# Optimization experiments

Measured on AMD Instinct MI355X. Metric: run time of the kernel, lower is better.

The kernel has to match this reference:

```python
import jax, jax.numpy as jnp
import numpy as np

MARGIN = 0.2
ENCODER_STRIDE = 320


def setup_inputs() -> dict:
    key = jax.random.key(0)
    k1, k2, k3, k4 = jax.random.split(key, 4)
    B, D, T, NC = 8, 512, 2048, 4096
    student_features = jax.random.normal(k1, (B, D, T), dtype=jnp.float32)
    codebook = jax.random.normal(k2, (NC, D), dtype=jnp.float32)
    teacher_codes = jax.random.randint(k3, (B, T), 0, NC, dtype=jnp.int64)
    lengths = jax.random.randint(k4, (B,), 0, T * ENCODER_STRIDE, dtype=jnp.int64)
    return {
        "student_features": student_features,
        "teacher_codes": teacher_codes,
        "codebook": codebook,
        "lengths": lengths,
    }


def reference(student_features, teacher_codes, codebook, lengths):
    B, D, T = student_features.shape
    # frame-level valid mask: (B, T)
    frame_lengths = lengths // ENCODER_STRIDE
    mask = (jnp.arange(T)[None, :] < frame_lengths[:, None]).astype(student_features.dtype)

    # (B*T, D) flattened student vectors
    z = jnp.transpose(student_features, (0, 2, 1)).reshape(-1, D)

    # Euclidean cdist via ||z||^2 + ||c||^2 - 2 z c^T (matmul form, like torch.cdist)
    sq = (
        jnp.sum(z * z, axis=-1, keepdims=True)
        + jnp.sum(codebook * codebook, axis=-1)[None, :]
        - 2.0 * jnp.einsum("nd,cd->nc", z, codebook)
    )
    dists = jnp.sqrt(jnp.maximum(sq, 1e-12))  # (B*T, num_codes)

    teacher_flat = teacher_codes.reshape(-1)
    rows = jnp.arange(teacher_flat.shape[0])
    pos_dist = dists[rows, teacher_flat]
    # exclude the target code, then min over codebook
    dists_for_neg = dists.at[rows, teacher_flat].set(jnp.inf)
    neg_dist = jnp.min(dists_for_neg, axis=1)

    triplet = jax.nn.relu(pos_dist.reshape(B, T) - neg_dist.reshape(B, T) + MARGIN)
    loss = jnp.sum(triplet * mask) / (jnp.sum(mask) + 1e-8)
    return loss
```

## Files before the change

kernel.cpp:

```cpp
#include <hip/hip_runtime.h>
#include <hip/hip_bf16.h>

typedef float f32x4 __attribute__((ext_vector_type(4)));
typedef int v8i __attribute__((ext_vector_type(8)));

#define NB 8
#define ND 512
#define NT 2048
#define NCODES 4096
#define NM (NB * NT)
#define MARGIN_F 0.2f
#define ENC_STRIDE 320


static __device__ inline bool rank_decode(const int* __restrict__ lengths, int rank,
                                          int shift, int& b, int& tib) {
    int acc = 0;
    bool ok = false;
#pragma unroll
    for (int bb = 0; bb < NB; bb++) {
        int fl = lengths[bb] / ENC_STRIDE;
        int c = (fl + ((1 << shift) - 1)) >> shift;
        if (!ok && rank < acc + c) { b = bb; tib = rank - acc; ok = true; }
        acc += c;
    }
    return ok;
}

__global__ void prep_fused(const float* __restrict__ sf, const float* __restrict__ cb,
                           const int* __restrict__ lengths,
                           unsigned char* __restrict__ Zq, float* __restrict__ npart,
                           unsigned char* __restrict__ Cq, float* __restrict__ cnorm,
                           float* __restrict__ accum, unsigned int* __restrict__ ticket) {
    __shared__ float tile[128][65];
    __shared__ float redc[4][16];
    const int tid = threadIdx.x;
    const int wave = tid >> 6, lane = tid & 63, l15 = lane & 15, kq = lane >> 4;

    if (blockIdx.x < 1024) {
        const int bx = blockIdx.x;
        int b, tt;
        if (!rank_decode(lengths, bx >> 2, 6, b, tt)) return;
        const int t0 = tt * 64;
        const int d0 = (bx & 3) * 128;
        const float* src = sf + (size_t)b * ND * NT;
#pragma unroll
        for (int it = 0; it < 8; it++) {
            int idx = it * 256 + tid;
            int d = idx >> 4, t4 = (idx & 15) * 4;
            float4 v = *(const float4*)(src + (size_t)(d0 + d) * NT + t0 + t4);
            tile[d][t4] = v.x; tile[d][t4 + 1] = v.y; tile[d][t4 + 2] = v.z; tile[d][t4 + 3] = v.w;
        }
        __syncthreads();
        const int m0 = b * NT + t0;
        {
            const int trow = wave * 16 + l15;
            unsigned char q[32];
#pragma unroll
            for (int j = 0; j < 32; j += 2) {
                float a = tile[kq * 32 + j][trow];
                float c = tile[kq * 32 + j + 1][trow];
                int p = __builtin_amdgcn_cvt_pk_fp8_f32(a, c, 0, false);
                q[j] = (unsigned char)(p & 0xFF);
                q[j + 1] = (unsigned char)((p >> 8) & 0xFF);
            }
            const int M_ = m0 >> 7, rg = ((m0 >> 4) & 7) + wave, K_ = d0 >> 7;
            char* base = (char*)Zq + ((size_t)((M_ * 4 + K_) * 8 + rg)) * 2048;
            *(uint4*)(base + lane * 16) = *(uint4*)&q[0];
            *(uint4*)(base + 1024 + lane * 16) = *(uint4*)&q[16];
        }
        if (tid < 64) {
            float s = 0.0f;
#pragma unroll 16
            for (int d = 0; d < 128; d++) {
                float v = tile[d][tid];
                s += v * v;
            }
            npart[(size_t)(d0 >> 7) * NM + m0 + tid] = s;
        }
    } else {
        if (blockIdx.x == 1279 && tid == 0) { *accum = 0.0f; *ticket = 0u; }
        const int r0 = (blockIdx.x - 1024) * 16;
        const int row = r0 + l15;
        const int K_ = wave;
        const float* src = cb + (size_t)row * ND + K_ * 128 + kq * 32;
        unsigned char q[32];
        float s = 0.0f;
#pragma unroll
        for (int j4 = 0; j4 < 8; j4++) {
            float4 v = *(const float4*)(src + j4 * 4);
            s += v.x * v.x + v.y * v.y + v.z * v.z + v.w * v.w;
            int p0 = __builtin_amdgcn_cvt_pk_fp8_f32(v.x, v.y, 0, false);
            int p1 = __builtin_amdgcn_cvt_pk_fp8_f32(v.z, v.w, 0, false);
            q[j4 * 4 + 0] = (unsigned char)(p0 & 0xFF);
            q[j4 * 4 + 1] = (unsigned char)((p0 >> 8) & 0xFF);
            q[j4 * 4 + 2] = (unsigned char)(p1 & 0xFF);
            q[j4 * 4 + 3] = (unsigned char)((p1 >> 8) & 0xFF);
        }
        const int N_ = r0 >> 7, rg = (r0 >> 4) & 7;
        char* base = (char*)Cq + ((size_t)((N_ * 4 + K_) * 8 + rg)) * 2048;
        *(uint4*)(base + lane * 16) = *(uint4*)&q[0];
        *(uint4*)(base + 1024 + lane * 16) = *(uint4*)&q[16];
        s += __shfl_xor(s, 16);
        s += __shfl_xor(s, 32);
        if (lane < 16) redc[wave][l15] = s;
        __syncthreads();
        if (tid < 16) cnorm[r0 + tid] = redc[0][tid] + redc[1][tid] + redc[2][tid] + redc[3][tid];
    }
}

__global__ __launch_bounds__(256, 2) void triplet_main(
    const unsigned char* __restrict__ Zq, const unsigned char* __restrict__ Cq,
    const float* __restrict__ cnorm, const int* __restrict__ teacher,
    const int* __restrict__ lengths,
    float* __restrict__ negq, float* __restrict__ posq) {
    int b, tM;
    if (!rank_decode(lengths, (int)blockIdx.x >> 3, 7, b, tM)) return;
    const int nq = blockIdx.x & 7;
    const int M_ = b * 16 + tM;
    const int m0 = M_ * 128;

    const int tid = threadIdx.x;
    const int wave = tid >> 6, lane = tid & 63;
    const int wr = wave >> 1, wc = wave & 1;
    const int l15 = lane & 15, quad = lane >> 4;

    const float INF = __builtin_inff();
    float minv[4][4], posv[4][4];
    int tch[4][4];
#pragma unroll
    for (int mi = 0; mi < 4; mi++)
#pragma unroll
        for (int r = 0; r < 4; r++) {
            minv[mi][r] = INF;
            posv[mi][r] = INF;
            tch[mi][r] = teacher[m0 + wr * 64 + mi * 16 + quad * 4 + r];
        }

    const char* gA = (const char*)Zq + (size_t)(M_ * 4) * 16384 + (wr * 4) * 2048 + lane * 16;
    const char* gB = (const char*)Cq + (size_t)(nq * 16) * 16384 + (wc * 4) * 2048 + lane * 16;

#pragma unroll 1
    for (int nt = 0; nt < 4; ++nt) {
        f32x4 acc[4][4];
#pragma unroll
        for (int mi = 0; mi < 4; mi++)
#pragma unroll
            for (int ni = 0; ni < 4; ni++)
                acc[mi][ni] = (f32x4){0.f, 0.f, 0.f, 0.f};

#pragma unroll 1
        for (int kt = 0; kt < 4; ++kt) {
            const char* pA = gA + (size_t)kt * 16384;
            const char* pB = gB + (size_t)(nt * 4 + kt) * 16384;
            v8i av[4], bv[4];
#pragma unroll
            for (int mi = 0; mi < 4; mi++) {
                union { uint4 q[2]; v8i v; } uu;
                uu.q[0] = *(const uint4*)(pA + mi * 2048);
                uu.q[1] = *(const uint4*)(pA + mi * 2048 + 1024);
                av[mi] = uu.v;
            }
#pragma unroll
            for (int ni = 0; ni < 4; ni++) {
                union { uint4 q[2]; v8i v; } uu;
                uu.q[0] = *(const uint4*)(pB + ni * 2048);
                uu.q[1] = *(const uint4*)(pB + ni * 2048 + 1024);
                bv[ni] = uu.v;
            }
#pragma unroll
            for (int mi = 0; mi < 4; mi++)
#pragma unroll
                for (int ni = 0; ni < 4; ni++)
                    acc[mi][ni] = __builtin_amdgcn_mfma_scale_f32_16x16x128_f8f6f4(
                        av[mi], bv[ni], acc[mi][ni], 0, 0,
                        0, 0x7F7F7F7F, 0, 0x7F7F7F7F);
        }

        const int n0 = (nq * 4 + nt) * 128;
        float cn[4]; int col[4];
#pragma unroll
        for (int ni = 0; ni < 4; ni++) {
            col[ni] = n0 + wc * 64 + ni * 16 + l15;
            cn[ni] = cnorm[col[ni]];
        }
#pragma unroll
        for (int mi = 0; mi < 4; mi++)
#pragma unroll
            for (int r = 0; r < 4; r++) {
                int t = tch[mi][r];
#pragma unroll
                for (int ni = 0; ni < 4; ni++) {
                    float val = fmaf(-2.0f, acc[mi][ni][r], cn[ni]);
                    bool ist = (col[ni] == t);
                    minv[mi][r] = fminf(minv[mi][r], ist ? INF : val);
                    posv[mi][r] = fminf(posv[mi][r], ist ? val : INF);
                }
            }
    }

    const int slot = nq * 2 + wc;
#pragma unroll
    for (int mi = 0; mi < 4; mi++)
#pragma unroll
        for (int r = 0; r < 4; r++) {
            float mn = minv[mi][r], ps = posv[mi][r];
#pragma unroll
            for (int off = 1; off < 16; off <<= 1) {
                mn = fminf(mn, __shfl_xor(mn, off));
                ps = fminf(ps, __shfl_xor(ps, off));
            }
            if (l15 == 0) {
                int m = m0 + wr * 64 + mi * 16 + quad * 4 + r;
                negq[(size_t)slot * NM + m] = mn;
                posq[(size_t)slot * NM + m] = ps;
            }
        }
}

__global__ void reduce_final(const float* __restrict__ negq, const float* __restrict__ posq,
                             const float* __restrict__ npart, const int* __restrict__ lengths,
                             float* __restrict__ accum, unsigned int* __restrict__ ticket,
                             float* __restrict__ out) {
    const float INF = __builtin_inff();
    const int m = blockIdx.x * 256 + threadIdx.x;
    float mn = INF, ps = INF;
#pragma unroll
    for (int s = 0; s < 16; s++) {
        mn = fminf(mn, negq[(size_t)s * NM + m]);
        ps = fminf(ps, posq[(size_t)s * NM + m]);
    }
    float zn = npart[m] + npart[NM + m] + npart[2 * NM + m] + npart[3 * NM + m];
    float negd = sqrtf(fmaxf(zn + mn, 1e-12f));
    float posd = sqrtf(fmaxf(zn + ps, 1e-12f));
    float tri = fmaxf(posd - negd + MARGIN_F, 0.0f);
    int b = m >> 11;
    int tt = m & (NT - 1);
    int flen = lengths[b] / ENC_STRIDE;
    float val = (tt < flen) ? tri : 0.0f;

    __shared__ float red[4];
#pragma unroll
    for (int off = 1; off < 64; off <<= 1) val += __shfl_xor(val, off);
    int lane = threadIdx.x & 63, w = threadIdx.x >> 6;
    if (lane == 0) red[w] = val;
    __syncthreads();
    if (threadIdx.x == 0) {
        atomicAdd(accum, red[0] + red[1] + red[2] + red[3]);
        __threadfence();
        unsigned int old = atomicAdd(ticket, 1u);
        if (old == 63u) {
            float total = atomicAdd(accum, 0.0f);
            float cnt = 0.0f;
            for (int bb = 0; bb < NB; bb++) cnt += (float)(lengths[bb] / ENC_STRIDE);
            out[0] = total / (cnt + 1e-8f);
        }
    }
}

extern "C" void kernel_launch(void* const* d_in, const int* in_sizes, int n_in,
                              void* d_out, int out_size, void* d_ws, size_t ws_size,
                              hipStream_t stream) {
    const float* sf = (const float*)d_in[0];
    const int* teacher = (const int*)d_in[1];
    const float* cb = (const float*)d_in[2];
    const int* lengths = (const int*)d_in[3];

    char* ws = (char*)d_ws;
    unsigned char* Zq = (unsigned char*)(ws);
    unsigned char* Cq = (unsigned char*)(ws + 8388608);
    float* cnorm = (float*)(ws + 10485760);
    float* npart = (float*)(ws + 10502144);
    float* negq = (float*)(ws + 10764288);
    float* posq = (float*)(ws + 11812864);
    float* accum = (float*)(ws + 12861440);
    unsigned int* ticket = (unsigned int*)(ws + 12861444);

    prep_fused<<<1280, 256, 0, stream>>>(sf, cb, lengths, Zq, npart, Cq, cnorm, accum, ticket);
    triplet_main<<<1024, 256, 0, stream>>>(Zq, Cq, cnorm, teacher, lengths, negq, posq);
    reduce_final<<<64, 256, 0, stream>>>(negq, posq, npart, lengths, accum, ticket,
                                         (float*)d_out);
}
```

Before: 134.7 us.

## Double-buffer fp8 fragment loads in registers and swizzle block-to-tile mapping

Replaces the serial load-then-MFMA k-loop with a register double-buffered pipeline. The next k-slice of A and B fragments is fetched while MFMAs run on the current slice, and the prefetch crosses the nt boundary. The block index is also remapped so that 8 consecutive blocks cover different M tiles sharing the same codebook quarter, which is meant to improve L2 reuse of the codebook. Holding two fragment sets raises register pressure, which risks spills or lower occupancy under launch_bounds(256,2).

```diff
diff --git a/kernel.cpp b/kernel.cpp
--- a/kernel.cpp
+++ b/kernel.cpp
@@ -109,14 +109,45 @@
     }
 }
 
+static __device__ inline v8i ldfrag(const char* p) {
+    union { uint4 q[2]; v8i v; } u;
+    u.q[0] = *(const uint4*)p;
+    u.q[1] = *(const uint4*)(p + 1024);
+    return u.v;
+}
+
+static __device__ inline void load_frags(const char* gA, const char* gB, int u,
+                                         v8i* av, v8i* bv) {
+    const char* pA = gA + (size_t)(u & 3) * 16384;
+    const char* pB = gB + (size_t)u * 16384;
+#pragma unroll
+    for (int i = 0; i < 4; i++) av[i] = ldfrag(pA + i * 2048);
+#pragma unroll
+    for (int i = 0; i < 4; i++) bv[i] = ldfrag(pB + i * 2048);
+}
+
+static __device__ inline void mfma16(const v8i* av, const v8i* bv, f32x4 (*acc)[4]) {
+#pragma unroll
+    for (int mi = 0; mi < 4; mi++)
+#pragma unroll
+        for (int ni = 0; ni < 4; ni++)
+            acc[mi][ni] = __builtin_amdgcn_mfma_scale_f32_16x16x128_f8f6f4(
+                av[mi], bv[ni], acc[mi][ni], 0, 0,
+                0, 0x7F7F7F7F, 0, 0x7F7F7F7F);
+}
+
 __global__ __launch_bounds__(256, 2) void triplet_main(
     const unsigned char* __restrict__ Zq, const unsigned char* __restrict__ Cq,
     const float* __restrict__ cnorm, const int* __restrict__ teacher,
     const int* __restrict__ lengths,
     float* __restrict__ negq, float* __restrict__ posq) {
+    const int blk = (int)blockIdx.x;
+    const int x = blk & 7;
+    const int j = blk >> 3;
+    const int m_rank = x + 8 * (j >> 3);
+    const int nq = j & 7;
     int b, tM;
-    if (!rank_decode(lengths, (int)blockIdx.x >> 3, 7, b, tM)) return;
-    const int nq = blockIdx.x & 7;
+    if (!rank_decode(lengths, m_rank, 7, b, tM)) return;
     const int M_ = b * 16 + tM;
     const int m0 = M_ * 128;
 
@@ -140,8 +171,12 @@
     const char* gA = (const char*)Zq + (size_t)(M_ * 4) * 16384 + (wr * 4) * 2048 + lane * 16;
     const char* gB = (const char*)Cq + (size_t)(nq * 16) * 16384 + (wc * 4) * 2048 + lane * 16;
 
+    v8i a0[4], b0[4], a1[4], b1[4];
+    load_frags(gA, gB, 0, a0, b0);
+
 #pragma unroll 1
     for (int nt = 0; nt < 4; ++nt) {
+        const int u0 = nt * 4;
         f32x4 acc[4][4];
 #pragma unroll
         for (int mi = 0; mi < 4; mi++)
@@ -149,33 +184,14 @@
             for (int ni = 0; ni < 4; ni++)
                 acc[mi][ni] = (f32x4){0.f, 0.f, 0.f, 0.f};
 
-#pragma unroll 1
-        for (int kt = 0; kt < 4; ++kt) {
-            const char* pA = gA + (size_t)kt * 16384;
-            const char* pB = gB + (size_t)(nt * 4 + kt) * 16384;
-            v8i av[4], bv[4];
-#pragma unroll
-            for (int mi = 0; mi < 4; mi++) {
-                union { uint4 q[2]; v8i v; } uu;
-                uu.q[0] = *(const uint4*)(pA + mi * 2048);
-                uu.q[1] = *(const uint4*)(pA + mi * 2048 + 1024);
-                av[mi] = uu.v;
-            }
-#pragma unroll
-            for (int ni = 0; ni < 4; ni++) {
-                union { uint4 q[2]; v8i v; } uu;
-                uu.q[0] = *(const uint4*)(pB + ni * 2048);
-                uu.q[1] = *(const uint4*)(pB + ni * 2048 + 1024);
-                bv[ni] = uu.v;
-            }
-#pragma unroll
-            for (int mi = 0; mi < 4; mi++)
-#pragma unroll
-                for (int ni = 0; ni < 4; ni++)
-                    acc[mi][ni] = __builtin_amdgcn_mfma_scale_f32_16x16x128_f8f6f4(
-                        av[mi], bv[ni], acc[mi][ni], 0, 0,
-                        0, 0x7F7F7F7F, 0, 0x7F7F7F7F);
-        }
+        load_frags(gA, gB, u0 + 1, a1, b1);
+        mfma16(a0, b0, acc);
+        load_frags(gA, gB, u0 + 2, a0, b0);
+        mfma16(a1, b1, acc);
+        load_frags(gA, gB, u0 + 3, a1, b1);
+        mfma16(a0, b0, acc);
+        if (nt < 3) load_frags(gA, gB, u0 + 4, a0, b0);
+        mfma16(a1, b1, acc);
 
         const int n0 = (nq * 4 + nt) * 128;
         float cn[4]; int col[4];
```

Measured after the change: 322.1 us. 139% more time.
